# Kernel optimization log

Measured on AMD Instinct MI355X. Metric: run time of the kernel, lower is better.

Reference implementation:

```python
import jax, jax.numpy as jnp
import numpy as np

B, CLS, C, H, HP, WP, K = 16, 20, 512, 4, 32, 32, 9
G = H * CLS  # grapher channels = 80
EPS = 1e-5
BNS = 1.0 / np.sqrt(1.0 + EPS)  # eval-mode BN, running_mean=0, running_var=1


def _bn(x, g, b, axis):
    shape = [1] * x.ndim
    shape[axis] = -1
    return x * (g * BNS).reshape(shape) + b.reshape(shape)


def setup_inputs():
    key = jax.random.key(0)
    ks = jax.random.split(key, 16)
    def rn(k, shp, scale=0.02):
        return jax.random.normal(k, shp, dtype=jnp.float32) * scale
    return {
        "x_cls": jax.random.normal(ks[0], (B, CLS, C), jnp.float32),
        "x_patch": jax.random.normal(ks[1], (B, C, HP, WP), jnp.float32),
        "norm_x_w": jnp.ones((C, 1, 1), jnp.float32),
        "norm_x_b": jnp.zeros((C, 1, 1), jnp.float32),
        "pq_w": rn(ks[2], (C, C)), "pq_b": rn(ks[3], (C,)),
        "ncls_w": jnp.ones((C,), jnp.float32), "ncls_b": jnp.zeros((C,), jnp.float32),
        "pkv_w": rn(ks[4], (2 * C, C)), "pkv_b": rn(ks[5], (2 * C,)),
        "fc1_w": rn(ks[6], (G, G)), "fc1_b": rn(ks[7], (G,)),
        "bn1_g": jnp.ones((G,), jnp.float32), "bn1_b": jnp.zeros((G,), jnp.float32),
        "mr_w": rn(ks[8], (2 * G, 2 * G // H)), "mr_b": rn(ks[9], (2 * G,)),
        "bn2_g": jnp.ones((2 * G,), jnp.float32), "bn2_b": jnp.zeros((2 * G,), jnp.float32),
        "fc2_w": rn(ks[10], (G, 2 * G)), "fc2_b": rn(ks[11], (G,)),
        "bn3_g": jnp.ones((G,), jnp.float32), "bn3_b": jnp.zeros((G,), jnp.float32),
        "proj_w": rn(ks[12], (C, C)), "proj_b": rn(ks[13], (C,)),
    }


def _forward(x_cls, x_patch, norm_x_w, norm_x_b, pq_w, pq_b, ncls_w, ncls_b,
             pkv_w, pkv_b, fc1_w, fc1_b, bn1_g, bn1_b, mr_w, mr_b, bn2_g, bn2_b,
             fc2_w, fc2_b, bn3_g, bn3_b, proj_w, proj_b):
    hd = C // H
    N = HP * WP
    scale = hd ** -0.5
    # norm_x: LayerNormGeneral over (C,H,W)
    c0 = x_patch - x_patch.mean(axis=(1, 2, 3), keepdims=True)
    s0 = (c0 * c0).mean(axis=(1, 2, 3), keepdims=True)
    xn = c0 / jnp.sqrt(s0 + EPS) * norm_x_w + norm_x_b
    # proj_q (1x1 conv) -> multi-head query [B,H,N,hd]
    q = jnp.einsum('oc,bchw->bohw', pq_w, xn) + pq_b[None, :, None, None]
    q = q.reshape(B, H, hd, N).transpose(0, 1, 3, 2)
    # norm_cls: LayerNorm over channel dim
    m = x_cls.mean(-1, keepdims=True)
    v = ((x_cls - m) ** 2).mean(-1, keepdims=True)
    xc = (x_cls - m) / jnp.sqrt(v + EPS) * ncls_w + ncls_b
    kv = xc @ pkv_w.T + pkv_b                                  # [B,Cls,2C]
    k_, v_ = kv[..., :C], kv[..., C:]
    key_ = k_.reshape(B, CLS, H, hd).transpose(0, 2, 3, 1)     # [B,H,hd,Cls]
    val = v_.reshape(B, CLS, H, hd).transpose(0, 2, 1, 3)      # [B,H,Cls,hd]
    attn = jnp.einsum('bhnd,bhdc->bhnc', q, key_) * scale      # [B,H,N,Cls]
    amap = attn.reshape(B, H, HP, WP, CLS).transpose(0, 1, 4, 2, 3).reshape(B, G, HP, WP)
    # ---- Grapher (ViG gcn_lib): fc1 -> DyGraphConv(MRConv, KNN) -> fc2 -> residual ----
    sc = amap
    x = jnp.einsum('oc,bchw->bohw', fc1_w, amap) + fc1_b[None, :, None, None]
    x = _bn(x, bn1_g, bn1_b, 1)
    xf = x.reshape(B, G, N).transpose(0, 2, 1)                 # [B,N,G]
    # dense KNN on L2-normalized features (indices only, non-diff)
    xu = xf / jnp.maximum(jnp.linalg.norm(xf, axis=-1, keepdims=True), 1e-12)
    sq = jnp.sum(xu * xu, axis=-1)                             # [B,N]
    neg_d = 2.0 * jnp.einsum('bnc,bmc->bnm', xu, xu) - sq[:, :, None] - sq[:, None, :]
    _, nn_idx = jax.lax.top_k(neg_d, K)                        # [B,N,K]
    neigh = xf[jnp.arange(B)[:, None, None], nn_idx]           # [B,N,K,G]
    xj = jnp.max(neigh - xf[:, :, None, :], axis=2)            # [B,N,G] max-relative
    y = jnp.stack([xf, xj], axis=-1).reshape(B, N, 2 * G)      # interleave (x0,xj0,x1,...)
    # grouped 1x1 conv (groups=H), BN, GELU
    yg = y.reshape(B, N, H, 2 * G // H)
    wg = mr_w.reshape(H, 2 * G // H, 2 * G // H)
    z = jnp.einsum('bngi,goi->bngo', yg, wg).reshape(B, N, 2 * G) + mr_b
    z = _bn(z, bn2_g, bn2_b, 2)
    z = jax.nn.gelu(z, approximate=False)
    z2 = z @ fc2_w.T + fc2_b                                   # [B,N,G]
    z2 = _bn(z2, bn3_g, bn3_b, 2)
    gout = z2.transpose(0, 2, 1).reshape(B, G, HP, WP) + sc
    # ---- softmax-weighted value aggregation ----
    attn2 = gout.reshape(B, H, CLS, N).transpose(0, 1, 3, 2)   # [B,H,N,Cls]
    attn2 = jax.nn.softmax(attn2, axis=-1)
    out = jnp.einsum('bhnc,bhcd->bhnd', attn2, val)            # [B,H,N,hd]
    out = out.transpose(0, 1, 3, 2).reshape(B, C, HP, WP)
    out = jnp.einsum('oc,bchw->bohw', proj_w, out) + proj_b[None, :, None, None]
    return x_patch + out


def reference(x_cls, x_patch, norm_x_w, norm_x_b, pq_w, pq_b, ncls_w, ncls_b,
              pkv_w, pkv_b, fc1_w, fc1_b, bn1_g, bn1_b, mr_w, mr_b, bn2_g, bn2_b,
              fc2_w, fc2_b, bn3_g, bn3_b, proj_w, proj_b):
    return _forward(x_cls, x_patch, norm_x_w, norm_x_b, pq_w, pq_b, ncls_w, ncls_b,
                    pkv_w, pkv_b, fc1_w, fc1_b, bn1_g, bn1_b, mr_w, mr_b, bn2_g, bn2_b,
                    fc2_w, fc2_b, bn3_g, bn3_b, proj_w, proj_b)
```

## Files before the change

kernel.cpp:

```cpp
#include <hip/hip_runtime.h>
#include <math.h>

#define DI __device__ __forceinline__

constexpr int B_ = 16, CLS_ = 20, C_ = 512, H_ = 4, HD_ = 128, N_ = 1024, G_ = 80, G2_ = 160, K_ = 9;
constexpr float EPS_ = 1e-5f;
constexpr float BNS_ = 0.9999950000374997f;
constexpr float SCALE_ = 0.08838834764831845f;
constexpr float INVSQRT2_ = 0.7071067811865475f;

typedef __attribute__((ext_vector_type(8))) short bf16x8;
typedef __attribute__((ext_vector_type(4))) float f32x4;

constexpr long OFF_PART  = 0;
constexpr long OFF_EB    = 4096;
constexpr long OFF_EBB   = OFF_EB    + 524288;
constexpr long OFF_KV    = OFF_EBB   + 2048;
constexpr long OFF_AMAPT = OFF_KV    + 327680;
constexpr long OFF_XF    = OFF_AMAPT + 1310720;
constexpr long OFF_XUB   = OFF_XF    + 1310720;
constexpr long OFF_W1BD  = OFF_XUB   + 786432;
constexpr long OFF_FC2B  = OFF_W1BD  + 16384;
constexpr long OFF_SQ    = OFF_FC2B  + 8192;
constexpr long OFF_NEGD  = OFF_SQ    + 16384;
constexpr long OFF_GOUTT = OFF_NEGD  + 16777216 + 147456;
constexpr long OFF_WPB   = OFF_GOUTT + 1310720;
constexpr long OFF_Y     = OFF_WPB   + 131072;
constexpr long OFF_FC1B  = OFF_Y     + 1310720;
constexpr long OFF_PB    = OFF_FC1B  + 4096;
constexpr long OFF_XCB   = OFF_PB    + 10240;
constexpr long OFF_PKVB  = OFF_XCB   + 131072;

DI float wsum(float v){
#pragma unroll
  for(int d=1; d<64; d<<=1) v += __shfl_xor(v, d);
  return v;
}
DI unsigned short f2b(float f){
  unsigned u = __float_as_uint(f);
  unsigned r = (u + 0x7FFFu + ((u >> 16) & 1u)) >> 16;
  return (unsigned short)r;
}

#define GLOAD16(g, s) __builtin_amdgcn_global_load_lds((const __attribute__((address_space(1))) void*)(g), \
                        (__attribute__((address_space(3))) void*)(s), 16, 0, 0)

__global__ __launch_bounds__(256) void k_pre(const float* __restrict__ x, float* __restrict__ part,
                                             const float* __restrict__ xcls,
                                             const float* __restrict__ ncw, const float* __restrict__ ncb,
                                             unsigned short* __restrict__ xcb,
                                             const float* __restrict__ pkvw, unsigned short* __restrict__ pkvb16,
                                             const float* __restrict__ projw, unsigned short* __restrict__ wpb,
                                             const float* __restrict__ mrw, const float* __restrict__ fc2w,
                                             const float* __restrict__ fc1w,
                                             unsigned short* __restrict__ w1bd, unsigned short* __restrict__ fc2b16,
                                             unsigned short* __restrict__ fc1b16){
  __shared__ float rs[4], rss[4];
  int blk = blockIdx.x, t = threadIdx.x;
  if(blk < 1024){
    const float4* xp = (const float4*)x;
    long base4 = (long)blk * 2048;
    float s = 0.f, ss = 0.f;
#pragma unroll
    for(int j=0;j<8;++j){
      float4 v = xp[base4 + t + 256*j];
      s  += v.x + v.y + v.z + v.w;
      ss += v.x*v.x + v.y*v.y + v.z*v.z + v.w*v.w;
    }
    s = wsum(s); ss = wsum(ss);
    int wv = t >> 6;
    if((t & 63) == 0){ rs[wv] = s; rss[wv] = ss; }
    __syncthreads();
    if(t == 0){
      part[blk*2]   = rs[0]+rs[1]+rs[2]+rs[3];
      part[blk*2+1] = rss[0]+rss[1]+rss[2]+rss[3];
    }
    return;
  }
  if(blk < 1040){
    int b = blk - 1024;
    int wv = t >> 6, l = t & 63;
    for(int cls = wv; cls < 32; cls += 4){
      unsigned short* orow = xcb + ((long)b*32 + cls)*512;
      if(cls < CLS_){
        const float* xr = xcls + ((long)b*CLS_ + cls) * C_;
        float vals[8];
        float s = 0.f, ss = 0.f;
#pragma unroll
        for(int j=0;j<8;++j){ float v = xr[l + 64*j]; vals[j] = v; s += v; ss += v*v; }
        s = wsum(s); ss = wsum(ss);
        float m = s / (float)C_;
        float var = ss / (float)C_ - m*m;
        float inv = 1.0f / sqrtf(var + EPS_);
#pragma unroll
        for(int j=0;j<8;++j){
          int c = l + 64*j;
          orow[c] = f2b((vals[j]-m)*inv*ncw[c] + ncb[c]);
        }
      } else {
#pragma unroll
        for(int j=0;j<8;++j) orow[l + 64*j] = 0;
      }
    }
    return;
  }
  if(blk < 1296){
    long i = (long)(blk - 1040)*256 + t;
    float4 v = ((const float4*)projw)[i];
    uint2 o;
    o.x = (unsigned)f2b(v.x) | ((unsigned)f2b(v.y) << 16);
    o.y = (unsigned)f2b(v.z) | ((unsigned)f2b(v.w) << 16);
    ((uint2*)wpb)[i] = o;
    return;
  }
  if(blk < 1808){
    long i = (long)(blk - 1296)*256 + t;
    float4 v = ((const float4*)pkvw)[i];
    uint2 o;
    o.x = (unsigned)f2b(v.x) | ((unsigned)f2b(v.y) << 16);
    o.y = (unsigned)f2b(v.z) | ((unsigned)f2b(v.w) << 16);
    ((uint2*)pkvb16)[i] = o;
    return;
  }
  int row = blk - 1808;
  if(row < 160){
    if(t < 160){
      unsigned short v = 0;
      if(t/40 == row/40) v = f2b(mrw[row*40 + (t % 40)]);
      w1bd[row*160 + t] = v;
    }
  } else if(row < 240){
    if(t < 160) fc2b16[(row-160)*160 + t] = f2b(fc2w[(long)(row-160)*160 + t]);
  } else if(row < 320){
    int r = row - 240;
    if(t < 96) fc1b16[r*96 + t] = (t < G_) ? f2b(fc1w[(long)r*G_ + t]) : (unsigned short)0;
  }
}

__global__ __launch_bounds__(256) void k_kv_mfma(const unsigned short* __restrict__ xcb,
                                                 const unsigned short* __restrict__ pkvb16,
                                                 const float* __restrict__ pkvb,
                                                 float* __restrict__ kv){
  __shared__ unsigned short Al[4096];
  __shared__ unsigned short Bl[1024];
  int b = blockIdx.x >> 3, o0 = (blockIdx.x & 7)*128;
  int t = threadIdx.x, w = t >> 6, l = t & 63;
  f32x4 acc[2][2] = {};
  const unsigned short* At = pkvb16 + (long)(o0 + w*16 + (l>>2))*512 + (l&3)*8;
  const unsigned short* Bt = xcb + ((long)b*32 + w*16 + (l>>2))*512 + (l&3)*8;
  int kq = (l >> 4)*8;
  for(int k0 = 0; k0 < 512; k0 += 32){
    if(k0) __syncthreads();
    GLOAD16(At + k0,          &Al[w*512]);
    GLOAD16(At + 64*512 + k0, &Al[2048 + w*512]);
    if(w < 2) GLOAD16(Bt + k0, &Bl[w*512]);
    __syncthreads();
    bf16x8 af[2], bfr[2];
#pragma unroll
    for(int mi=0; mi<2; ++mi) af[mi]  = *(const bf16x8*)&Al[(w*32 + mi*16 + (l & 15))*32 + kq];
#pragma unroll
    for(int ni=0; ni<2; ++ni) bfr[ni] = *(const bf16x8*)&Bl[(ni*16 + (l & 15))*32 + kq];
#pragma unroll
    for(int mi=0; mi<2; ++mi)
#pragma unroll
      for(int ni=0; ni<2; ++ni)
        acc[mi][ni] = __builtin_amdgcn_mfma_f32_16x16x32_bf16(af[mi], bfr[ni], acc[mi][ni], 0, 0, 0);
  }
  int r0 = (l >> 4)*4;
#pragma unroll
  for(int mi=0; mi<2; ++mi){
#pragma unroll
    for(int r=0; r<4; ++r){
      int o = o0 + w*32 + mi*16 + r0 + r;
      float bi = pkvb[o];
#pragma unroll
      for(int ni=0; ni<2; ++ni){
        int cls = ni*16 + (l & 15);
        if(cls < CLS_) kv[((long)b*CLS_ + cls)*1024 + o] = acc[mi][ni][r] + bi;
      }
    }
  }
}

__global__ __launch_bounds__(256) void k_eprep(const float* __restrict__ kv, const float* __restrict__ pqw,
                                               const float* __restrict__ pqb, const float* __restrict__ partbuf,
                                               const float* __restrict__ nw, const float* __restrict__ nbv,
                                               unsigned short* __restrict__ Eb, float* __restrict__ ebb,
                                               float* __restrict__ pb){
  int b = blockIdx.x, hh = blockIdx.y, cch = blockIdx.z, t = threadIdx.x;
  if(hh == 4){
    if(cch == 0){
      unsigned* z = (unsigned*)(Eb + ((long)b*128 + 80)*512);
      for(int i=t; i<12288; i+=256) z[i] = 0;
    }
    return;
  }
  __shared__ float sst[2];
  __shared__ float key[CLS_][HD_];
  __shared__ float part[4][CLS_][64];
  if(t < 64){
    float s  = partbuf[(b*64+t)*2];
    float ss = partbuf[(b*64+t)*2+1];
    s = wsum(s); ss = wsum(ss);
    if(t == 0){
      const float cnt = (float)(C_ * N_);
      float m = s / cnt;
      sst[0] = m;
      sst[1] = 1.0f / sqrtf(ss / cnt - m*m + EPS_);
    }
  }
  int h = hh, c0 = cch*64;
  for(int i=t; i<CLS_*HD_; i+=256){
    int cls = i >> 7, d = i & 127;
    key[cls][d] = kv[((long)b*CLS_+cls)*1024 + h*HD_ + d];
  }
  __syncthreads();
  float m = sst[0], inv = sst[1];
  int c = t & 63, ds = t >> 6;
  float acc[CLS_] = {};
  const float* wp = pqw + ((long)(h*HD_ + ds*32))*C_ + c0 + c;
#pragma unroll 8
  for(int di=0; di<32; ++di){
    float wv = wp[(long)di*C_];
#pragma unroll
    for(int cls=0; cls<CLS_; ++cls) acc[cls] += key[cls][ds*32+di]*wv;
  }
#pragma unroll
  for(int cls=0; cls<CLS_; ++cls) part[ds][cls][c] = acc[cls];
  __syncthreads();
  for(int i=t; i<CLS_*64; i+=256){
    int cls = i >> 6, cc = i & 63;
    float v = (part[0][cls][cc]+part[1][cls][cc]+part[2][cls][cc]+part[3][cls][cc]) * SCALE_;
    int cg = c0 + cc;
    float a = inv * nw[cg];
    float bbv = nbv[cg] - m*a;
    Eb[((long)b*128 + h*CLS_ + cls)*512 + cg] = f2b(v*a);
    part[0][cls][cc] = v*bbv;
  }
  __syncthreads();
  if(t < CLS_){
    float s = 0.f;
    for(int cc=0; cc<64; ++cc) s += part[0][t][cc];
    pb[((long)b*8 + cch)*G_ + h*CLS_ + t] = s;
  }
  if(cch == 0 && t >= 64 && t < 64 + CLS_){
    int tt = t - 64;
    float bacc = 0.f;
    for(int d=0; d<HD_; ++d) bacc += key[tt][d]*pqb[h*HD_+d];
    ebb[b*G_ + h*CLS_ + tt] = bacc*SCALE_;
  }
}

__global__ __launch_bounds__(256) void k_amap_fc1(const unsigned short* __restrict__ Eb,
                                                  const float* __restrict__ xp,
                                                  const float* __restrict__ ebb,
                                                  const float* __restrict__ pb,
                                                  const unsigned short* __restrict__ w1b,
                                                  const float* __restrict__ f1bias,
                                                  const float* __restrict__ g1, const float* __restrict__ b1,
                                                  float* __restrict__ amapT,
                                                  float* __restrict__ xf, unsigned short* __restrict__ xub,
                                                  float* __restrict__ sq){
  __shared__ unsigned short Xl[64*520];
  __shared__ unsigned short Bgl[4096];
  unsigned short* A1 = Xl;
  int b = blockIdx.y, n0 = blockIdx.x*64;
  int t = threadIdx.x, w = t >> 6, l = t & 63;
  int wr = w >> 1, wc = w & 1;
  {
    int nb = t & 7, cl = t >> 3;
    const float* xb = xp + (long)b*C_*N_ + n0 + nb*8;
#pragma unroll 4
    for(int pass=0; pass<16; ++pass){
      int c = pass*32 + cl;
      const float* src = xb + (long)c*N_;
      float4 v0 = *(const float4*)src;
      float4 v1 = *(const float4*)(src+4);
      int base = (nb*8)*520 + c;
      Xl[base         ] = f2b(v0.x);
      Xl[base + 520   ] = f2b(v0.y);
      Xl[base + 520*2 ] = f2b(v0.z);
      Xl[base + 520*3 ] = f2b(v0.w);
      Xl[base + 520*4 ] = f2b(v1.x);
      Xl[base + 520*5 ] = f2b(v1.y);
      Xl[base + 520*6 ] = f2b(v1.z);
      Xl[base + 520*7 ] = f2b(v1.w);
    }
  }
  __syncthreads();
  f32x4 acc[2][4] = {};
  const unsigned short* Bt = Eb + ((long)b*128 + w*16 + (l>>2))*512 + (l&3)*8;
  int ra = wr*32 + (l & 15);
  int rb = wc*64 + (l & 15);
  int kq = (l >> 4) * 8;
  for(int k0 = 0; k0 < 512; k0 += 32){
    if(k0) __syncthreads();
    GLOAD16(Bt + k0,          &Bgl[w*512]);
    GLOAD16(Bt + 64*512 + k0, &Bgl[2048 + w*512]);
    __syncthreads();
    bf16x8 af[2], bfr[4];
#pragma unroll
    for(int rt=0; rt<2; ++rt) af[rt]  = *(const bf16x8*)&Xl[(ra + rt*16)*520 + k0 + kq];
#pragma unroll
    for(int ct=0; ct<4; ++ct) bfr[ct] = *(const bf16x8*)&Bgl[(rb + ct*16)*32 + kq];
#pragma unroll
    for(int rt=0; rt<2; ++rt)
#pragma unroll
      for(int ct=0; ct<4; ++ct)
        acc[rt][ct] = __builtin_amdgcn_mfma_f32_16x16x32_bf16(af[rt], bfr[ct], acc[rt][ct], 0, 0, 0);
  }
  float bias4[4];
#pragma unroll
  for(int ct=0; ct<4; ++ct){
    int g = wc*64 + ct*16 + (l & 15);
    float bi = 0.f;
    if(g < G_){
      bi = ebb[b*G_ + g];
#pragma unroll
      for(int cc=0; cc<8; ++cc) bi += pb[((long)b*8 + cc)*G_ + g];
    }
    bias4[ct] = bi;
  }
  __syncthreads();
  int r0 = (l >> 4)*4;
#pragma unroll
  for(int rt=0; rt<2; ++rt){
#pragma unroll
    for(int r=0; r<4; ++r){
      int lrow = wr*32 + rt*16 + r0 + r;
      long rowb = ((long)b*N_ + n0 + lrow)*G_;
#pragma unroll
      for(int ct=0; ct<4; ++ct){
        int g = wc*64 + ct*16 + (l & 15);
        if(g < G_){
          float val = acc[rt][ct][r] + bias4[ct];
          amapT[rowb + g] = val;
          A1[lrow*96 + g] = f2b(val);
        } else if(g < 96){
          A1[lrow*96 + g] = 0;
        }
      }
    }
  }
  __syncthreads();
  int lr = l & 15, lk = l >> 4;
  bf16x8 ay[3];
  const unsigned short* arow = &A1[(w*16 + lr)*96 + lk*8];
#pragma unroll
  for(int ks=0; ks<3; ++ks) ay[ks] = *(const bf16x8*)&arow[ks*32];
  f32x4 acc5[5] = {};
  const unsigned short* wrow = w1b + (long)lr*96 + lk*8;
#pragma unroll
  for(int ks=0; ks<3; ++ks){
#pragma unroll
    for(int ct=0; ct<5; ++ct){
      bf16x8 bw = *(const bf16x8*)&wrow[ct*16*96 + ks*32];
      acc5[ct] = __builtin_amdgcn_mfma_f32_16x16x32_bf16(ay[ks], bw, acc5[ct], 0, 0, 0);
    }
  }
  float v[5][4];
  float ssq[4] = {0.f,0.f,0.f,0.f};
#pragma unroll
  for(int ct=0; ct<5; ++ct){
    int o = ct*16 + lr;
    float bi = f1bias[o], ga = g1[o]*BNS_, bb = b1[o];
#pragma unroll
    for(int i=0;i<4;++i){
      float vv = (acc5[ct][i] + bi)*ga + bb;
      v[ct][i] = vv;
      ssq[i] += vv*vv;
    }
  }
#pragma unroll
  for(int d=1; d<16; d<<=1){
#pragma unroll
    for(int i=0;i<4;++i) ssq[i] += __shfl_xor(ssq[i], d);
  }
  long row0g = (long)b*N_ + n0 + w*16;
#pragma unroll
  for(int i=0;i<4;++i){
    long row = row0g + lk*4 + i;
    float invn = 1.0f / fmaxf(sqrtf(ssq[i]), 1e-12f);
#pragma unroll
    for(int ct=0; ct<5; ++ct){
      int o = ct*16 + lr;
      xf[row*G_ + o] = v[ct][i];
      xub[row*96 + o] = f2b(v[ct][i]*invn);
    }
    xub[row*96 + 80 + lr] = 0;
    if(lr == 0) sq[row] = ssq[i]*invn*invn;
  }
}

template<bool RES>
__global__ __launch_bounds__(256) void k_gemm_mfma(const unsigned short* __restrict__ Wb,
                                                   const unsigned short* __restrict__ Xb,
                                                   const float* __restrict__ bias,
                                                   const float* __restrict__ Res,
                                                   float* __restrict__ Out){
  __shared__ unsigned short Al[4096];
  __shared__ unsigned short Bl[4096];
  int b = blockIdx.z;
  int o0 = blockIdx.y*128, n0 = blockIdx.x*128;
  int t = threadIdx.x, w = t >> 6, l = t & 63;
  int wr = w >> 1, wc = w & 1;
  f32x4 acc[4][4] = {};
  const unsigned short* Wt = Wb + (long)(o0 + w*16 + (l>>2))*512 + (l&3)*8;
  const unsigned short* Xt = Xb + ((long)b*N_ + n0 + w*16 + (l>>2))*512 + (l&3)*8;
  int ra = wr*64 + (l & 15);
  int rb = wc*64 + (l & 15);
  int kq = (l >> 4) * 8;
  for(int k0 = 0; k0 < 512; k0 += 32){
    if(k0) __syncthreads();
    GLOAD16(Wt + k0,            &Al[w*512]);
    GLOAD16(Wt + 64*512 + k0,   &Al[2048 + w*512]);
    GLOAD16(Xt + k0,            &Bl[w*512]);
    GLOAD16(Xt + 64*512 + k0,   &Bl[2048 + w*512]);
    __syncthreads();
    bf16x8 af[4], bfr[4];
#pragma unroll
    for(int i=0;i<4;++i){
      af[i]  = *(const bf16x8*)&Al[(ra + i*16)*32 + kq];
      bfr[i] = *(const bf16x8*)&Bl[(rb + i*16)*32 + kq];
    }
#pragma unroll
    for(int mi=0; mi<4; ++mi)
#pragma unroll
      for(int ni=0; ni<4; ++ni)
        acc[mi][ni] = __builtin_amdgcn_mfma_f32_16x16x32_bf16(af[mi], bfr[ni], acc[mi][ni], 0, 0, 0);
  }
  long obase = ((long)b*C_ + o0 + wr*64)*N_ + n0 + wc*64 + (l & 15);
  int r0 = (l >> 4) * 4;
#pragma unroll
  for(int mi=0; mi<4; ++mi){
#pragma unroll
    for(int r=0; r<4; ++r){
      int row = mi*16 + r0 + r;
      float bi = bias[o0 + wr*64 + row];
#pragma unroll
      for(int ni=0; ni<4; ++ni){
        long oi = obase + (long)row*N_ + ni*16;
        float v = acc[mi][ni][r] + bi;
        if(RES) v += Res[oi];
        Out[oi] = v;
      }
    }
  }
}

__global__ __launch_bounds__(256) void k_negd_mfma(const unsigned short* __restrict__ xub,
                                                   const float* __restrict__ sq,
                                                   float* __restrict__ negd){
  __shared__ unsigned short Al[128*96];
  __shared__ unsigned short Bl[128*96];
  int b = blockIdx.z;
  int n0 = blockIdx.y*128, m0 = blockIdx.x*128;
  int t = threadIdx.x, w = t >> 6, l = t & 63;
  int wr = w >> 1, wc = w & 1;
  const unsigned short* gA = xub + ((long)b*N_ + n0)*96;
  const unsigned short* gB = xub + ((long)b*N_ + m0)*96;
#pragma unroll
  for(int rd=0; rd<6; ++rd){
    int chunk = rd*4 + w;
    GLOAD16(gA + chunk*512 + l*8, &Al[chunk*512]);
    GLOAD16(gB + chunk*512 + l*8, &Bl[chunk*512]);
  }
  __syncthreads();
  f32x4 acc[4][4] = {};
  int ra = wr*64 + (l & 15);
  int rb = wc*64 + (l & 15);
#pragma unroll
  for(int ks=0; ks<3; ++ks){
    int kq = ks*32 + (l >> 4)*8;
    bf16x8 af[4], bfr[4];
#pragma unroll
    for(int i=0;i<4;++i){
      af[i]  = *(const bf16x8*)&Al[(ra + i*16)*96 + kq];
      bfr[i] = *(const bf16x8*)&Bl[(rb + i*16)*96 + kq];
    }
#pragma unroll
    for(int mi=0; mi<4; ++mi)
#pragma unroll
      for(int ni=0; ni<4; ++ni)
        acc[mi][ni] = __builtin_amdgcn_mfma_f32_16x16x32_bf16(af[mi], bfr[ni], acc[mi][ni], 0, 0, 0);
  }
  int r0 = (l >> 4)*4;
  const float* sqb = sq + (long)b*N_;
#pragma unroll
  for(int mi=0; mi<4; ++mi){
#pragma unroll
    for(int r=0; r<4; ++r){
      int n = n0 + wr*64 + mi*16 + r0 + r;
      float sn = sqb[n];
      long row = ((long)b*N_ + n)*N_;
#pragma unroll
      for(int ni=0; ni<4; ++ni){
        int m = m0 + wc*64 + ni*16 + (l & 15);
        negd[row + m] = 2.f*acc[mi][ni][r] - sn - sqb[m];
      }
    }
  }
}

__global__ __launch_bounds__(256) void k_topk_y(const float* __restrict__ negd, const float* __restrict__ xf,
                                                unsigned short* __restrict__ y){
  int t = threadIdx.x, wv = t >> 6, l = t & 63;
  long r = (long)blockIdx.x*4 + wv;
  long b = r >> 10;
  const float* row = negd + r*N_;
  float vals[16];
#pragma unroll
  for(int j=0;j<16;++j) vals[j] = row[l + 64*j];
  int nbs[K_];
#pragma unroll
  for(int p=0; p<K_; ++p){
    float bv = vals[0]; int bj = 0;
#pragma unroll
    for(int j=1;j<16;++j) if(vals[j] > bv){ bv = vals[j]; bj = j; }
    int bm = l + 64*bj;
#pragma unroll
    for(int d=1; d<64; d<<=1){
      float ov = __shfl_xor(bv, d);
      int   om = __shfl_xor(bm, d);
      if(ov > bv || (ov == bv && om < bm)){ bv = ov; bm = om; }
    }
    nbs[p] = bm;
#pragma unroll
    for(int j=0;j<16;++j) if(bm == l + 64*j) vals[j] = -INFINITY;
  }
  const float* frow = xf + r*G_;
  int o2s = (l < 16) ? (64 + l) : 0;
  float f0 = frow[l];
  float f1 = frow[o2s];
  float m0 = -INFINITY, m1 = -INFINITY;
#pragma unroll
  for(int k=0;k<K_;++k){
    const float* nr = xf + ((long)b*N_ + nbs[k])*G_;
    m0 = fmaxf(m0, nr[l]);
    m1 = fmaxf(m1, nr[o2s]);
  }
  unsigned short* yr = y + r*G2_;
  ushort2 u0; u0.x = f2b(f0); u0.y = f2b(m0 - f0);
  *(ushort2*)&yr[2*l] = u0;
  if(l < 16){
    ushort2 u1; u1.x = f2b(f1); u1.y = f2b(m1 - f1);
    *(ushort2*)&yr[128 + 2*l] = u1;
  }
}

__global__ __launch_bounds__(256) void k_mixer_mfma(const unsigned short* __restrict__ y,
                                                    const unsigned short* __restrict__ w1bd,
                                                    const float* __restrict__ mrb,
                                                    const float* __restrict__ g2, const float* __restrict__ b2,
                                                    const unsigned short* __restrict__ fc2b16,
                                                    const float* __restrict__ fc2bias,
                                                    const float* __restrict__ g3, const float* __restrict__ b3,
                                                    const float* __restrict__ amapT, float* __restrict__ goutT){
  __shared__ unsigned short zl[4][16][G2_];
  int t = threadIdx.x, w = t >> 6, l = t & 63;
  long row0 = ((long)blockIdx.x*4 + w)*16;
  int lr = l & 15, lk = l >> 4;
  bf16x8 ay[5];
  const unsigned short* yrow = y + (row0 + lr)*G2_ + lk*8;
#pragma unroll
  for(int ks=0; ks<5; ++ks) ay[ks] = *(const bf16x8*)&yrow[ks*32];
  f32x4 accz[10] = {};
  const unsigned short* wb = w1bd + (long)lr*G2_ + lk*8;
#pragma unroll
  for(int ks=0; ks<5; ++ks){
#pragma unroll
    for(int ct=0; ct<10; ++ct){
      bf16x8 bw = *(const bf16x8*)&wb[ct*16*G2_ + ks*32];
      accz[ct] = __builtin_amdgcn_mfma_f32_16x16x32_bf16(ay[ks], bw, accz[ct], 0, 0, 0);
    }
  }
#pragma unroll
  for(int ct=0; ct<10; ++ct){
    int o = ct*16 + lr;
    float bi = mrb[o], ga = g2[o]*BNS_, bb = b2[o];
#pragma unroll
    for(int i=0;i<4;++i){
      float v = (accz[ct][i] + bi)*ga + bb;
      float zz = v * 0.5f * (1.0f + erff(v * INVSQRT2_));
      zl[w][lk*4 + i][o] = f2b(zz);
    }
  }
  __syncthreads();
  bf16x8 az[5];
#pragma unroll
  for(int ks=0; ks<5; ++ks) az[ks] = *(const bf16x8*)&zl[w][lr][ks*32 + lk*8];
  f32x4 acc2[5] = {};
  const unsigned short* fb = fc2b16 + (long)lr*G2_ + lk*8;
#pragma unroll
  for(int ks=0; ks<5; ++ks){
#pragma unroll
    for(int ct=0; ct<5; ++ct){
      bf16x8 bw = *(const bf16x8*)&fb[ct*16*G2_ + ks*32];
      acc2[ct] = __builtin_amdgcn_mfma_f32_16x16x32_bf16(az[ks], bw, acc2[ct], 0, 0, 0);
    }
  }
#pragma unroll
  for(int ct=0; ct<5; ++ct){
    int o = ct*16 + lr;
    float bi = fc2bias[o], ga = g3[o]*BNS_, bb = b3[o];
#pragma unroll
    for(int i=0;i<4;++i){
      long row = row0 + lk*4 + i;
      float v = (acc2[ct][i] + bi)*ga + bb + amapT[row*G_ + o];
      goutT[row*G_ + o] = v;
    }
  }
}

__global__ __launch_bounds__(256) void k_softmax_pv(const float* __restrict__ goutT, const float* __restrict__ kv,
                                                    unsigned short* __restrict__ aob){
  int bh = blockIdx.x; int b = bh >> 2, h = bh & 3;
  int n0 = blockIdx.y * 64;
  __shared__ unsigned short Vt[128*32];
  __shared__ unsigned short Pl[64*40];
  __shared__ unsigned short Os[64*132];
  int t = threadIdx.x, w = t >> 6, l = t & 63;
  if(t < 128){
    int d = t;
    const float* vb = kv + ((long)b*CLS_)*1024 + C_ + h*HD_ + d;
#pragma unroll
    for(int cls=0; cls<CLS_; ++cls) Vt[d*32+cls] = f2b(vb[(long)cls*1024]);
#pragma unroll
    for(int cls=CLS_; cls<32; ++cls) Vt[d*32+cls] = 0;
  }
  if(t < 64){
    int n = n0 + t;
    const float* gr = goutT + ((long)b*N_ + n)*G_ + h*CLS_;
    float x[CLS_];
    float mx = -INFINITY;
#pragma unroll
    for(int cls=0; cls<CLS_; ++cls){ x[cls] = gr[cls]; mx = fmaxf(mx, x[cls]); }
    float s = 0.f;
#pragma unroll
    for(int cls=0; cls<CLS_; ++cls){ x[cls] = expf(x[cls]-mx); s += x[cls]; }
    float inv = 1.0f / s;
#pragma unroll
    for(int cls=0; cls<CLS_; ++cls) Pl[t*40+cls] = f2b(x[cls]*inv);
#pragma unroll
    for(int cls=CLS_; cls<32; ++cls) Pl[t*40+cls] = 0;
  }
  __syncthreads();
  int lr = l & 15, kq = (l >> 4)*8;
  f32x4 acc[4][2] = {};
  bf16x8 af[4], bf2[2];
#pragma unroll
  for(int rt=0; rt<4; ++rt) af[rt] = *(const bf16x8*)&Pl[(rt*16+lr)*40 + kq];
#pragma unroll
  for(int ci=0; ci<2; ++ci) bf2[ci] = *(const bf16x8*)&Vt[((2*w+ci)*16+lr)*32 + kq];
#pragma unroll
  for(int rt=0; rt<4; ++rt)
#pragma unroll
    for(int ci=0; ci<2; ++ci)
      acc[rt][ci] = __builtin_amdgcn_mfma_f32_16x16x32_bf16(af[rt], bf2[ci], acc[rt][ci], 0, 0, 0);
  int r0 = (l >> 4)*4;
#pragma unroll
  for(int rt=0; rt<4; ++rt)
#pragma unroll
    for(int ci=0; ci<2; ++ci)
#pragma unroll
      for(int i=0; i<4; ++i)
        Os[(rt*16 + r0 + i)*132 + (2*w+ci)*16 + lr] = f2b(acc[rt][ci][i]);
  __syncthreads();
  unsigned short* ob = aob + ((long)b*N_ + n0)*C_ + h*HD_;
#pragma unroll
  for(int j=0; j<8; ++j){
    int idx = t + 256*j;
    int row = idx >> 5, ch = idx & 31;
    *(ushort4*)&ob[(long)row*C_ + ch*4] =
        *(const ushort4*)&Os[row*132 + ch*4];
  }
}

extern "C" void kernel_launch(void* const* d_in, const int* in_sizes, int n_in,
                              void* d_out, int out_size, void* d_ws, size_t ws_size,
                              hipStream_t stream){
  const float* x_cls   = (const float*)d_in[0];
  const float* x_patch = (const float*)d_in[1];
  const float* norm_x_w = (const float*)d_in[2];
  const float* norm_x_b = (const float*)d_in[3];
  const float* pq_w  = (const float*)d_in[4];
  const float* pq_b  = (const float*)d_in[5];
  const float* ncls_w = (const float*)d_in[6];
  const float* ncls_b = (const float*)d_in[7];
  const float* pkv_w = (const float*)d_in[8];
  const float* pkv_b = (const float*)d_in[9];
  const float* fc1_w = (const float*)d_in[10];
  const float* fc1_b = (const float*)d_in[11];
  const float* bn1_g = (const float*)d_in[12];
  const float* bn1_b = (const float*)d_in[13];
  const float* mr_w  = (const float*)d_in[14];
  const float* mr_b  = (const float*)d_in[15];
  const float* bn2_g = (const float*)d_in[16];
  const float* bn2_b = (const float*)d_in[17];
  const float* fc2_w = (const float*)d_in[18];
  const float* fc2_b = (const float*)d_in[19];
  const float* bn3_g = (const float*)d_in[20];
  const float* bn3_b = (const float*)d_in[21];
  const float* proj_w = (const float*)d_in[22];
  const float* proj_b = (const float*)d_in[23];

  float* ws = (float*)d_ws;
  float* part   = ws + OFF_PART;
  float* ebb    = ws + OFF_EBB;
  float* kvbuf  = ws + OFF_KV;
  float* amapT  = ws + OFF_AMAPT;
  float* xf     = ws + OFF_XF;
  float* sqbuf  = ws + OFF_SQ;
  float* negd   = ws + OFF_NEGD;
  float* goutT  = ws + OFF_GOUTT;
  float* pbuf   = ws + OFF_PB;
  unsigned short* Eb     = (unsigned short*)(ws + OFF_EB);
  unsigned short* xub    = (unsigned short*)(ws + OFF_XUB);
  unsigned short* w1bd   = (unsigned short*)(ws + OFF_W1BD);
  unsigned short* fc2b16 = (unsigned short*)(ws + OFF_FC2B);
  unsigned short* ybuf   = (unsigned short*)(ws + OFF_Y);
  unsigned short* fc1b16 = (unsigned short*)(ws + OFF_FC1B);
  unsigned short* xcb    = (unsigned short*)(ws + OFF_XCB);
  unsigned short* pkvb16 = (unsigned short*)(ws + OFF_PKVB);
  unsigned short* aob = (unsigned short*)(ws + OFF_NEGD);
  unsigned short* wpb = (unsigned short*)(ws + OFF_WPB);
  float* out = (float*)d_out;

  k_pre<<<2128, 256, 0, stream>>>(x_patch, part, x_cls, ncls_w, ncls_b, xcb,
                                  pkv_w, pkvb16, proj_w, wpb,
                                  mr_w, fc2_w, fc1_w, w1bd, fc2b16, fc1b16);
  k_kv_mfma<<<128, 256, 0, stream>>>(xcb, pkvb16, pkv_b, kvbuf);
  k_eprep<<<dim3(16,5,8), 256, 0, stream>>>(kvbuf, pq_w, pq_b, part, norm_x_w, norm_x_b, Eb, ebb, pbuf);
  k_amap_fc1<<<dim3(16,16), 256, 0, stream>>>(Eb, x_patch, ebb, pbuf, fc1b16, fc1_b, bn1_g, bn1_b,
                                              amapT, xf, xub, sqbuf);
  k_negd_mfma<<<dim3(8,8,16), 256, 0, stream>>>(xub, sqbuf, negd);
  k_topk_y<<<4096, 256, 0, stream>>>(negd, xf, ybuf);
  k_mixer_mfma<<<256, 256, 0, stream>>>(ybuf, w1bd, mr_b, bn2_g, bn2_b,
                                        fc2b16, fc2_b, bn3_g, bn3_b, amapT, goutT);
  k_softmax_pv<<<dim3(64,16), 256, 0, stream>>>(goutT, kvbuf, aob);
  k_gemm_mfma<true><<<dim3(8,4,16), 256, 0, stream>>>(wpb, aob, proj_b, x_patch, out);
}
```

Measured before the change: 162.3 us.

## Fuse grapher mixer with softmax and value aggregation into one kernel

Merges the mixer MFMA kernel and the softmax/PV kernel so each 64-row block keeps its gout tile in shared memory, computes softmax for all four heads, and multiplies by V for every head in-block. This removes the goutT workspace round trip and one kernel launch. In exchange, each block rebuilds the full bf16 V table for all heads (more redundant loads per block), uses more LDS per block (lower occupancy), and writes output directly with scattered 2-byte stores instead of staged vectorized stores. Softmax runs on only 16 lanes per wave, serialized over heads.

```diff
diff --git a/kernel.cpp b/kernel.cpp
--- a/kernel.cpp
+++ b/kernel.cpp
@@ -23,8 +23,7 @@
 constexpr long OFF_FC2B  = OFF_W1BD  + 16384;
 constexpr long OFF_SQ    = OFF_FC2B  + 8192;
 constexpr long OFF_NEGD  = OFF_SQ    + 16384;
-constexpr long OFF_GOUTT = OFF_NEGD  + 16777216 + 147456;
-constexpr long OFF_WPB   = OFF_GOUTT + 1310720;
+constexpr long OFF_WPB   = OFF_NEGD  + 16777216 + 147456;
 constexpr long OFF_Y     = OFF_WPB   + 131072;
 constexpr long OFF_FC1B  = OFF_Y     + 1310720;
 constexpr long OFF_PB    = OFF_FC1B  + 4096;
@@ -548,18 +547,30 @@
   }
 }
 
-__global__ __launch_bounds__(256) void k_mixer_mfma(const unsigned short* __restrict__ y,
+__global__ __launch_bounds__(256) void k_mixer_attn(const unsigned short* __restrict__ y,
                                                     const unsigned short* __restrict__ w1bd,
                                                     const float* __restrict__ mrb,
                                                     const float* __restrict__ g2, const float* __restrict__ b2,
                                                     const unsigned short* __restrict__ fc2b16,
                                                     const float* __restrict__ fc2bias,
                                                     const float* __restrict__ g3, const float* __restrict__ b3,
-                                                    const float* __restrict__ amapT, float* __restrict__ goutT){
-  __shared__ unsigned short zl[4][16][G2_];
+                                                    const float* __restrict__ amapT, const float* __restrict__ kv,
+                                                    unsigned short* __restrict__ aob){
+  __shared__ unsigned short Vt[4*128*32];
+  __shared__ float Gl[64][85];
+  __shared__ unsigned short zp[10240];
   int t = threadIdx.x, w = t >> 6, l = t & 63;
-  long row0 = ((long)blockIdx.x*4 + w)*16;
+  int blk = blockIdx.x;
+  int b = blk >> 4;
+  long row0 = (long)blk*64 + w*16;
   int lr = l & 15, lk = l >> 4;
+
+  for(int i = t; i < 4*128*32; i += 256){
+    int h = i >> 12, rem = i & 4095, d = rem >> 5, cls = rem & 31;
+    Vt[i] = (cls < CLS_) ? f2b(kv[((long)b*CLS_ + cls)*1024 + C_ + h*HD_ + d]) : (unsigned short)0;
+  }
+
+  unsigned short (*zl)[16][G2_] = (unsigned short(*)[16][G2_])zp;
   bf16x8 ay[5];
   const unsigned short* yrow = y + (row0 + lr)*G2_ + lk*8;
 #pragma unroll
@@ -605,74 +616,60 @@
     float bi = fc2bias[o], ga = g3[o]*BNS_, bb = b3[o];
 #pragma unroll
     for(int i=0;i<4;++i){
-      long row = row0 + lk*4 + i;
-      float v = (acc2[ct][i] + bi)*ga + bb + amapT[row*G_ + o];
-      goutT[row*G_ + o] = v;
-    }
-  }
-}
-
-__global__ __launch_bounds__(256) void k_softmax_pv(const float* __restrict__ goutT, const float* __restrict__ kv,
-                                                    unsigned short* __restrict__ aob){
-  int bh = blockIdx.x; int b = bh >> 2, h = bh & 3;
-  int n0 = blockIdx.y * 64;
-  __shared__ unsigned short Vt[128*32];
-  __shared__ unsigned short Pl[64*40];
-  __shared__ unsigned short Os[64*132];
-  int t = threadIdx.x, w = t >> 6, l = t & 63;
-  if(t < 128){
-    int d = t;
-    const float* vb = kv + ((long)b*CLS_)*1024 + C_ + h*HD_ + d;
-#pragma unroll
-    for(int cls=0; cls<CLS_; ++cls) Vt[d*32+cls] = f2b(vb[(long)cls*1024]);
-#pragma unroll
-    for(int cls=CLS_; cls<32; ++cls) Vt[d*32+cls] = 0;
-  }
-  if(t < 64){
-    int n = n0 + t;
-    const float* gr = goutT + ((long)b*N_ + n)*G_ + h*CLS_;
-    float x[CLS_];
-    float mx = -INFINITY;
-#pragma unroll
-    for(int cls=0; cls<CLS_; ++cls){ x[cls] = gr[cls]; mx = fmaxf(mx, x[cls]); }
-    float s = 0.f;
-#pragma unroll
-    for(int cls=0; cls<CLS_; ++cls){ x[cls] = expf(x[cls]-mx); s += x[cls]; }
-    float inv = 1.0f / s;
-#pragma unroll
-    for(int cls=0; cls<CLS_; ++cls) Pl[t*40+cls] = f2b(x[cls]*inv);
-#pragma unroll
-    for(int cls=CLS_; cls<32; ++cls) Pl[t*40+cls] = 0;
-  }
-  __syncthreads();
-  int lr = l & 15, kq = (l >> 4)*8;
-  f32x4 acc[4][2] = {};
-  bf16x8 af[4], bf2[2];
-#pragma unroll
-  for(int rt=0; rt<4; ++rt) af[rt] = *(const bf16x8*)&Pl[(rt*16+lr)*40 + kq];
-#pragma unroll
-  for(int ci=0; ci<2; ++ci) bf2[ci] = *(const bf16x8*)&Vt[((2*w+ci)*16+lr)*32 + kq];
-#pragma unroll
-  for(int rt=0; rt<4; ++rt)
-#pragma unroll
-    for(int ci=0; ci<2; ++ci)
-      acc[rt][ci] = __builtin_amdgcn_mfma_f32_16x16x32_bf16(af[rt], bf2[ci], acc[rt][ci], 0, 0, 0);
-  int r0 = (l >> 4)*4;
-#pragma unroll
-  for(int rt=0; rt<4; ++rt)
-#pragma unroll
-    for(int ci=0; ci<2; ++ci)
-#pragma unroll
-      for(int i=0; i<4; ++i)
-        Os[(rt*16 + r0 + i)*132 + (2*w+ci)*16 + lr] = f2b(acc[rt][ci][i]);
-  __syncthreads();
-  unsigned short* ob = aob + ((long)b*N_ + n0)*C_ + h*HD_;
-#pragma unroll
-  for(int j=0; j<8; ++j){
-    int idx = t + 256*j;
-    int row = idx >> 5, ch = idx & 31;
-    *(ushort4*)&ob[(long)row*C_ + ch*4] =
-        *(const ushort4*)&Os[row*132 + ch*4];
+      int lrow = w*16 + lk*4 + i;
+      long grow = row0 + lk*4 + i;
+      Gl[lrow][o] = (acc2[ct][i] + bi)*ga + bb + amapT[grow*G_ + o];
+    }
+  }
+  __syncthreads();
+
+  unsigned short* Pl = zp;
+  if(l < 16){
+    int lrow = w*16 + lr;
+#pragma unroll
+    for(int h=0; h<4; ++h){
+      float x[CLS_];
+      float mx = -INFINITY;
+#pragma unroll
+      for(int cls=0; cls<CLS_; ++cls){ x[cls] = Gl[lrow][h*CLS_ + cls]; mx = fmaxf(mx, x[cls]); }
+      float s = 0.f;
+#pragma unroll
+      for(int cls=0; cls<CLS_; ++cls){ x[cls] = expf(x[cls]-mx); s += x[cls]; }
+      float inv = 1.0f / s;
+      unsigned short* pr = &Pl[((long)h*64 + lrow)*40];
+#pragma unroll
+      for(int cls=0; cls<CLS_; ++cls) pr[cls] = f2b(x[cls]*inv);
+#pragma unroll
+      for(int cls=CLS_; cls<32; ++cls) pr[cls] = 0;
+    }
+  }
+  __syncthreads();
+
+  int kq = lk*8, r0 = lk*4;
+  unsigned short* ob = aob + (long)blk*64*C_;
+#pragma unroll
+  for(int h=0; h<4; ++h){
+    bf16x8 af[4], bf2[2];
+#pragma unroll
+    for(int rt=0; rt<4; ++rt) af[rt] = *(const bf16x8*)&Pl[((long)h*64 + rt*16 + lr)*40 + kq];
+#pragma unroll
+    for(int ci=0; ci<2; ++ci) bf2[ci] = *(const bf16x8*)&Vt[h*4096 + ((2*w+ci)*16 + lr)*32 + kq];
+    f32x4 acc[4][2] = {};
+#pragma unroll
+    for(int rt=0; rt<4; ++rt)
+#pragma unroll
+      for(int ci=0; ci<2; ++ci)
+        acc[rt][ci] = __builtin_amdgcn_mfma_f32_16x16x32_bf16(af[rt], bf2[ci], acc[rt][ci], 0, 0, 0);
+#pragma unroll
+    for(int rt=0; rt<4; ++rt)
+#pragma unroll
+      for(int ci=0; ci<2; ++ci)
+#pragma unroll
+        for(int i=0; i<4; ++i){
+          int lrow = rt*16 + r0 + i;
+          int d = h*HD_ + (2*w+ci)*16 + lr;
+          ob[(long)lrow*C_ + d] = f2b(acc[rt][ci][i]);
+        }
   }
 }
 
@@ -712,7 +709,6 @@
   float* xf     = ws + OFF_XF;
   float* sqbuf  = ws + OFF_SQ;
   float* negd   = ws + OFF_NEGD;
-  float* goutT  = ws + OFF_GOUTT;
   float* pbuf   = ws + OFF_PB;
   unsigned short* Eb     = (unsigned short*)(ws + OFF_EB);
   unsigned short* xub    = (unsigned short*)(ws + OFF_XUB);
@@ -735,8 +731,7 @@
                                               amapT, xf, xub, sqbuf);
   k_negd_mfma<<<dim3(8,8,16), 256, 0, stream>>>(xub, sqbuf, negd);
   k_topk_y<<<4096, 256, 0, stream>>>(negd, xf, ybuf);
-  k_mixer_mfma<<<256, 256, 0, stream>>>(ybuf, w1bd, mr_b, bn2_g, bn2_b,
-                                        fc2b16, fc2_b, bn3_g, bn3_b, amapT, goutT);
-  k_softmax_pv<<<dim3(64,16), 256, 0, stream>>>(goutT, kvbuf, aob);
+  k_mixer_attn<<<256, 256, 0, stream>>>(ybuf, w1bd, mr_b, bn2_g, bn2_b,
+                                        fc2b16, fc2_b, bn3_g, bn3_b, amapT, kvbuf, aob);
   k_gemm_mfma<true><<<dim3(8,4,16), 256, 0, stream>>>(wpb, aob, proj_b, x_patch, out);
 }
```

Result: slower. 174.0 us (+7.2%).

## Fuse partial top-k into distance GEMM epilogue and merge candidates

Applied to the files above, without the earlier changes.

The distance GEMM no longer writes the full BxNxN fp32 negative-distance matrix. Instead, each wave computes a per-row top-9 over its 64-column tile using 16-lane shuffles and writes 9 (value, index) candidates per tile. A lighter merge kernel then picks the final 9 neighbours from the 144 candidates per row. This removes a 64MB write and read round-trip to memory, at the cost of extra shuffle work in the GEMM epilogue and a new candidate buffer.

```diff
diff --git a/kernel.cpp b/kernel.cpp
--- a/kernel.cpp
+++ b/kernel.cpp
@@ -22,8 +22,9 @@
 constexpr long OFF_W1BD  = OFF_XUB   + 786432;
 constexpr long OFF_FC2B  = OFF_W1BD  + 16384;
 constexpr long OFF_SQ    = OFF_FC2B  + 8192;
-constexpr long OFF_NEGD  = OFF_SQ    + 16384;
-constexpr long OFF_GOUTT = OFF_NEGD  + 16777216 + 147456;
+constexpr long OFF_CAND  = OFF_SQ    + 16384;
+constexpr long OFF_AOB   = OFF_CAND  + 4718592;
+constexpr long OFF_GOUTT = OFF_AOB   + 4194304;
 constexpr long OFF_WPB   = OFF_GOUTT + 1310720;
 constexpr long OFF_Y     = OFF_WPB   + 131072;
 constexpr long OFF_FC1B  = OFF_Y     + 1310720;
@@ -448,9 +449,9 @@
   }
 }
 
-__global__ __launch_bounds__(256) void k_negd_mfma(const unsigned short* __restrict__ xub,
+__global__ __launch_bounds__(256) void k_negd_cand(const unsigned short* __restrict__ xub,
                                                    const float* __restrict__ sq,
-                                                   float* __restrict__ negd){
+                                                   float2* __restrict__ cand){
   __shared__ unsigned short Al[128*96];
   __shared__ unsigned short Bl[128*96];
   int b = blockIdx.z;
@@ -484,40 +485,65 @@
       for(int ni=0; ni<4; ++ni)
         acc[mi][ni] = __builtin_amdgcn_mfma_f32_16x16x32_bf16(af[mi], bfr[ni], acc[mi][ni], 0, 0, 0);
   }
-  int r0 = (l >> 4)*4;
+  int lk = l >> 4, lm = l & 15;
+  int mbase = m0 + wc*64 + lm;
   const float* sqb = sq + (long)b*N_;
+  float smv[4];
+#pragma unroll
+  for(int ni=0; ni<4; ++ni) smv[ni] = sqb[m0 + wc*64 + ni*16 + lm];
+  int ht = blockIdx.x*2 + wc;
 #pragma unroll
   for(int mi=0; mi<4; ++mi){
 #pragma unroll
     for(int r=0; r<4; ++r){
-      int n = n0 + wr*64 + mi*16 + r0 + r;
+      int n = n0 + wr*64 + mi*16 + lk*4 + r;
       float sn = sqb[n];
-      long row = ((long)b*N_ + n)*N_;
-#pragma unroll
-      for(int ni=0; ni<4; ++ni){
-        int m = m0 + wc*64 + ni*16 + (l & 15);
-        negd[row + m] = 2.f*acc[mi][ni][r] - sn - sqb[m];
+      float key[4];
+#pragma unroll
+      for(int ni=0; ni<4; ++ni) key[ni] = 2.f*acc[mi][ni][r] - sn - smv[ni];
+      long cbase = (((long)b*N_ + n)*16 + ht)*9;
+#pragma unroll
+      for(int p=0; p<K_; ++p){
+        float bv = key[0]; int bj = 0;
+#pragma unroll
+        for(int j=1;j<4;++j) if(key[j] > bv){ bv = key[j]; bj = j; }
+        int bm = mbase + bj*16;
+#pragma unroll
+        for(int d=1; d<16; d<<=1){
+          float ov = __shfl_xor(bv, d);
+          int   om = __shfl_xor(bm, d);
+          if(ov > bv || (ov == bv && om < bm)){ bv = ov; bm = om; }
+        }
+        if(lm == p){
+          float2 cd; cd.x = bv; cd.y = __int_as_float(bm);
+          cand[cbase + p] = cd;
+        }
+#pragma unroll
+        for(int j=0;j<4;++j) if(bm == mbase + j*16) key[j] = -INFINITY;
       }
     }
   }
 }
 
-__global__ __launch_bounds__(256) void k_topk_y(const float* __restrict__ negd, const float* __restrict__ xf,
-                                                unsigned short* __restrict__ y){
+__global__ __launch_bounds__(256) void k_merge_y(const float2* __restrict__ cand, const float* __restrict__ xf,
+                                                 unsigned short* __restrict__ y){
   int t = threadIdx.x, wv = t >> 6, l = t & 63;
   long r = (long)blockIdx.x*4 + wv;
   long b = r >> 10;
-  const float* row = negd + r*N_;
-  float vals[16];
-#pragma unroll
-  for(int j=0;j<16;++j) vals[j] = row[l + 64*j];
+  const float2* cr = cand + r*144;
+  float cv[3]; int ci[3];
+  {
+    float2 c0 = cr[l];        cv[0] = c0.x; ci[0] = __float_as_int(c0.y);
+    float2 c1 = cr[l + 64];   cv[1] = c1.x; ci[1] = __float_as_int(c1.y);
+    if(l < 16){ float2 c2 = cr[l + 128]; cv[2] = c2.x; ci[2] = __float_as_int(c2.y); }
+    else      { cv[2] = -INFINITY; ci[2] = 0x7FFFFFFF; }
+  }
   int nbs[K_];
 #pragma unroll
   for(int p=0; p<K_; ++p){
-    float bv = vals[0]; int bj = 0;
-#pragma unroll
-    for(int j=1;j<16;++j) if(vals[j] > bv){ bv = vals[j]; bj = j; }
-    int bm = l + 64*bj;
+    float bv = cv[0]; int bm = ci[0];
+    if(cv[1] > bv || (cv[1] == bv && ci[1] < bm)){ bv = cv[1]; bm = ci[1]; }
+    if(cv[2] > bv || (cv[2] == bv && ci[2] < bm)){ bv = cv[2]; bm = ci[2]; }
 #pragma unroll
     for(int d=1; d<64; d<<=1){
       float ov = __shfl_xor(bv, d);
@@ -526,7 +552,7 @@
     }
     nbs[p] = bm;
 #pragma unroll
-    for(int j=0;j<16;++j) if(bm == l + 64*j) vals[j] = -INFINITY;
+    for(int j=0;j<3;++j) if(ci[j] == bm) cv[j] = -INFINITY;
   }
   const float* frow = xf + r*G_;
   int o2s = (l < 16) ? (64 + l) : 0;
@@ -711,9 +737,9 @@
   float* amapT  = ws + OFF_AMAPT;
   float* xf     = ws + OFF_XF;
   float* sqbuf  = ws + OFF_SQ;
-  float* negd   = ws + OFF_NEGD;
   float* goutT  = ws + OFF_GOUTT;
   float* pbuf   = ws + OFF_PB;
+  float2* candb = (float2*)(ws + OFF_CAND);
   unsigned short* Eb     = (unsigned short*)(ws + OFF_EB);
   unsigned short* xub    = (unsigned short*)(ws + OFF_XUB);
   unsigned short* w1bd   = (unsigned short*)(ws + OFF_W1BD);
@@ -722,7 +748,7 @@
   unsigned short* fc1b16 = (unsigned short*)(ws + OFF_FC1B);
   unsigned short* xcb    = (unsigned short*)(ws + OFF_XCB);
   unsigned short* pkvb16 = (unsigned short*)(ws + OFF_PKVB);
-  unsigned short* aob = (unsigned short*)(ws + OFF_NEGD);
+  unsigned short* aob = (unsigned short*)(ws + OFF_AOB);
   unsigned short* wpb = (unsigned short*)(ws + OFF_WPB);
   float* out = (float*)d_out;
 
@@ -733,8 +759,8 @@
   k_eprep<<<dim3(16,5,8), 256, 0, stream>>>(kvbuf, pq_w, pq_b, part, norm_x_w, norm_x_b, Eb, ebb, pbuf);
   k_amap_fc1<<<dim3(16,16), 256, 0, stream>>>(Eb, x_patch, ebb, pbuf, fc1b16, fc1_b, bn1_g, bn1_b,
                                               amapT, xf, xub, sqbuf);
-  k_negd_mfma<<<dim3(8,8,16), 256, 0, stream>>>(xub, sqbuf, negd);
-  k_topk_y<<<4096, 256, 0, stream>>>(negd, xf, ybuf);
+  k_negd_cand<<<dim3(8,8,16), 256, 0, stream>>>(xub, sqbuf, candb);
+  k_merge_y<<<4096, 256, 0, stream>>>(candb, xf, ybuf);
   k_mixer_mfma<<<256, 256, 0, stream>>>(ybuf, w1bd, mr_b, bn2_g, bn2_b,
                                         fc2b16, fc2_b, bn3_g, bn3_b, amapT, goutT);
   k_softmax_pv<<<dim3(64,16), 256, 0, stream>>>(goutT, kvbuf, aob);
```

Result: slower. 270.6 us (+66.8%).
